# Performance work log

Measured on AMD Instinct MI355X. Metric: run time of the kernel, lower is better.

The kernel has to match this reference:

```python
import jax, jax.numpy as jnp
import numpy as np
import math

B, T = 32768, 34
VOCAB = 14
SQRT_HD = math.sqrt(3.0)

def _pos_flat_index():
    # flatten (source, index) pairs into indices of a [14,3] table:
    # rows 0-9 = digit spiral enc, row 10 = z10_enc, rows 11-13 = special_enc
    flat = []
    for p in range(34):
        if p < 10:
            flat.append(p)
        elif p == 10:
            flat.append(11 + 0)
        elif p < 21:
            flat.append(p - 11)
        elif p == 21:
            flat.append(11 + 1)
        elif p < 33:
            z = p - 22
            flat.append(z if z < 10 else 10)
        else:
            flat.append(11 + 2)
    return np.array(flat, dtype=np.int32)

POS_FLAT = _pos_flat_index()

def setup_inputs() -> dict:
    key = jax.random.key(0)
    ks = jax.random.split(key, 12)
    r = lambda k, s: jax.random.normal(k, s, dtype=jnp.float32)
    return {
        'idx': jax.random.randint(ks[0], (B, T), 0, VOCAB, dtype=jnp.int64),
        'tok_emb': r(ks[1], (14, 3)),
        'pos_params': r(ks[2], (4,)),
        'z10_enc': r(ks[3], (1, 3)),
        'special_enc': r(ks[4], (3, 3)),
        'wq': r(ks[5], (3, 6)), 'wk': r(ks[6], (3, 6)), 'wv': r(ks[7], (3, 6)),
        'wo': r(ks[8], (6, 6)),
        'ln1_g': jnp.ones(6), 'ln1_b': jnp.zeros(6),
        'ln2_g': jnp.ones(6), 'ln2_b': jnp.zeros(6),
        'lnf_g': jnp.ones(6), 'lnf_b': jnp.zeros(6),
        'ffn_w1': r(ks[9], (6, 2)), 'ffn_b1': jnp.zeros(2),
        'ffn_w2': r(ks[10], (2, 6)), 'ffn_b2': jnp.zeros(6),
        'head_w': r(ks[11], (6, 3)),
    }

def _ln(x, g, b):
    mu = x.mean(-1, keepdims=True)
    var = ((x - mu) ** 2).mean(-1, keepdims=True)
    return (x - mu) * jax.lax.rsqrt(var + 1e-5) * g + b

def _forward(idx, tok_emb, pos_params, z10_enc, special_enc, wq, wk, wv, wo,
             ln1_g, ln1_b, ln2_g, ln2_b, lnf_g, lnf_b,
             ffn_w1, ffn_b1, ffn_w2, ffn_b2, head_w):
    amp, phase, slope, offset = pos_params[0], pos_params[1], pos_params[2], pos_params[3]
    i = jnp.arange(10, dtype=jnp.float32)
    ang = 2.0 * math.pi * i / 10.0 + phase
    digit = jnp.stack([amp * jnp.cos(ang), amp * jnp.sin(ang), slope * i + offset], -1)  # [10,3]
    table = jnp.concatenate([digit, z10_enc, special_enc], 0)  # [14,3]
    Tn = idx.shape[1]
    pos = table[POS_FLAT][:Tn]  # [T,3]
    tok = tok_emb[idx]  # [B,T,3]
    x = jnp.concatenate([tok, jnp.broadcast_to(pos, tok.shape)], -1)  # [B,T,6]
    h = _ln(x, ln1_g, ln1_b)
    h_tok, h_pos = h[..., :3], h[..., 3:]
    Bn = idx.shape[0]
    q = (h_pos @ wq).reshape(Bn, Tn, 2, 3)
    k = (h_pos @ wk).reshape(Bn, Tn, 2, 3)
    v = (h_tok @ wv).reshape(Bn, Tn, 2, 3)
    attn = jnp.einsum('bqhd,bkhd->bhqk', q, k) / SQRT_HD
    mask = jnp.tril(jnp.ones((Tn, Tn), bool))
    attn = jax.nn.softmax(jnp.where(mask, attn, -jnp.inf), axis=-1)
    o = jnp.einsum('bhqk,bkhd->bqhd', attn, v).reshape(Bn, Tn, 6)
    x = x + o @ wo
    h2 = _ln(x, ln2_g, ln2_b)
    x = x + (jax.nn.gelu(h2 @ ffn_w1 + ffn_b1, approximate=False) @ ffn_w2 + ffn_b2)
    x = _ln(x, lnf_g, lnf_b)
    return (x @ head_w) @ tok_emb.T  # [B,T,14]

def reference(idx, tok_emb, pos_params, z10_enc, special_enc, wq, wk, wv, wo,
              ln1_g, ln1_b, ln2_g, ln2_b, lnf_g, lnf_b,
              ffn_w1, ffn_b1, ffn_w2, ffn_b2, head_w):
    return _forward(idx, tok_emb, pos_params, z10_enc, special_enc, wq, wk, wv, wo,
                    ln1_g, ln1_b, ln2_g, ln2_b, lnf_g, lnf_b,
                    ffn_w1, ffn_b1, ffn_w2, ffn_b2, head_w)
```

## Files before the change

### kernel.cpp

```cpp
#include <hip/hip_runtime.h>
#include <math.h>

#define BT    34
#define TPR   17
#define RPB   15
#define BLOCK 256

typedef float v2f __attribute__((ext_vector_type(2)));
typedef float v4f __attribute__((ext_vector_type(4)));

#define QSCALE 0.83294037332470f

#if __has_builtin(__builtin_amdgcn_exp2f)
#define EXP2(x) __builtin_amdgcn_exp2f(x)
#else
#define EXP2(x) exp2f(x)
#endif

__device__ __forceinline__ void ln6(const float* x, const float* g, const float* b, float* o) {
  float mu = (x[0]+x[1]+x[2]+x[3]+x[4]+x[5]) * (1.0f/6.0f);
  float v = 0.f;
  #pragma unroll
  for (int c = 0; c < 6; ++c) { float d = x[c]-mu; v += d*d; }
  float inv = rsqrtf(v * (1.0f/6.0f) + 1e-5f);
  #pragma unroll
  for (int c = 0; c < 6; ++c) o[c] = (x[c]-mu)*inv*g[c] + b[c];
}

__global__ __launch_bounds__(BLOCK, 4)
void addtrans_kernel(const int* __restrict__ idx,
                     const float* __restrict__ tok_emb,
                     const float* __restrict__ pos_params,
                     const float* __restrict__ z10_enc,
                     const float* __restrict__ special_enc,
                     const float* __restrict__ wq,
                     const float* __restrict__ wk,
                     const float* __restrict__ wv,
                     const float* __restrict__ wo,
                     const float* __restrict__ ln1_g, const float* __restrict__ ln1_b,
                     const float* __restrict__ ln2_g, const float* __restrict__ ln2_b,
                     const float* __restrict__ lnf_g, const float* __restrict__ lnf_b,
                     const float* __restrict__ ffn_w1, const float* __restrict__ ffn_b1,
                     const float* __restrict__ ffn_w2, const float* __restrict__ ffn_b2,
                     const float* __restrict__ head_w,
                     float* __restrict__ out, int B)
{
  __shared__ __align__(16) float s_mem[RPB*BT*14];
  __shared__ float s_te[42];
  __shared__ float s_pos[BT*3];
  __shared__ float s_wq[18], s_wk[18], s_wv[18], s_wo[36], s_hw[18];
  __shared__ float s_g1[6], s_b1[6], s_g2[6], s_b2[6], s_gf[6], s_bf[6];
  __shared__ float s_w1[12], s_w2[12], s_fb1[2], s_fb2[6];

  const int tid = threadIdx.x;

  if (tid < 42) s_te[tid] = tok_emb[tid];
  if (tid < 18) { s_wq[tid]=wq[tid]; s_wk[tid]=wk[tid]; s_wv[tid]=wv[tid]; s_hw[tid]=head_w[tid]; }
  if (tid < 36) s_wo[tid] = wo[tid];
  if (tid < 12) { s_w1[tid]=ffn_w1[tid]; s_w2[tid]=ffn_w2[tid]; }
  if (tid < 6)  { s_g1[tid]=ln1_g[tid]; s_b1[tid]=ln1_b[tid];
                  s_g2[tid]=ln2_g[tid]; s_b2[tid]=ln2_b[tid];
                  s_gf[tid]=lnf_g[tid]; s_bf[tid]=lnf_b[tid];
                  s_fb2[tid]=ffn_b2[tid]; }
  if (tid < 2)  s_fb1[tid] = ffn_b1[tid];
  if (tid < BT) {
    int p = tid, f;
    if (p < 10) f = p;
    else if (p == 10) f = 11;
    else if (p < 21) f = p - 11;
    else if (p == 21) f = 12;
    else if (p < 33) { int z = p - 22; f = (z < 10) ? z : 10; }
    else f = 13;
    float e0, e1, e2;
    if (f < 10) {
      float amp = pos_params[0], ph = pos_params[1], sl = pos_params[2], of = pos_params[3];
      float ang = 0.62831853071795864769f * (float)f + ph;
      e0 = amp * cosf(ang); e1 = amp * sinf(ang); e2 = sl * (float)f + of;
    } else if (f == 10) { e0 = z10_enc[0]; e1 = z10_enc[1]; e2 = z10_enc[2]; }
    else { int u = f - 11; e0 = special_enc[u*3]; e1 = special_enc[u*3+1]; e2 = special_enc[u*3+2]; }
    s_pos[tid*3+0] = e0; s_pos[tid*3+1] = e1; s_pos[tid*3+2] = e2;
  }
  __syncthreads();

  const int row = tid / TPR;
  const int j   = tid - row * TPR;
  const int b   = blockIdx.x * RPB + row;
  const bool active = (row < RPB) && (b < B);

  v2f   qp[2][3];
  float xr[2][6];

  if (active) {
    const int base = b * BT;
    #pragma unroll
    for (int s = 0; s < 2; ++s) {
      const int t = j + s * TPR;
      const int vid = idx[base + t];
      float x6[6];
      x6[0] = s_te[vid*3+0]; x6[1] = s_te[vid*3+1]; x6[2] = s_te[vid*3+2];
      x6[3] = s_pos[t*3+0];  x6[4] = s_pos[t*3+1];  x6[5] = s_pos[t*3+2];
      float h[6];
      ln6(x6, s_g1, s_b1, h);
      float q6[6], k6[6], v6[6];
      #pragma unroll
      for (int c = 0; c < 6; ++c) {
        q6[c] = h[3]*s_wq[c] + h[4]*s_wq[6+c] + h[5]*s_wq[12+c];
        k6[c] = h[3]*s_wk[c] + h[4]*s_wk[6+c] + h[5]*s_wk[12+c];
        v6[c] = h[0]*s_wv[c] + h[1]*s_wv[6+c] + h[2]*s_wv[12+c];
        xr[s][c] = x6[c];
      }
      qp[s][0] = (v2f){q6[0]*QSCALE, q6[3]*QSCALE};
      qp[s][1] = (v2f){q6[1]*QSCALE, q6[4]*QSCALE};
      qp[s][2] = (v2f){q6[2]*QSCALE, q6[5]*QSCALE};
      v4f* kvp = (v4f*)&s_mem[(row*BT + t)*12];
      kvp[0] = (v4f){k6[0], k6[3], k6[1], k6[4]};
      kvp[1] = (v4f){k6[2], k6[5], v6[0], v6[3]};
      kvp[2] = (v4f){v6[1], v6[4], v6[2], v6[5]};
    }
  }
  __syncthreads();

  v2f l0 = (v2f){0.f,0.f}, l1 = (v2f){0.f,0.f};
  v2f o0[3] = {(v2f){0.f,0.f},(v2f){0.f,0.f},(v2f){0.f,0.f}};
  v2f o1[3] = {(v2f){0.f,0.f},(v2f){0.f,0.f},(v2f){0.f,0.f}};
  if (active) {
    const v4f* kvb = (const v4f*)&s_mem[row * (BT*12)];
    #pragma unroll 4
    for (int k = 0; k < TPR; ++k) {
      v4f A = kvb[k*3+0], Bv = kvb[k*3+1], C = kvb[k*3+2];
      v2f kA = (v2f){A.x, A.y}, kB = (v2f){A.z, A.w}, kC = (v2f){Bv.x, Bv.y};
      v2f vA = (v2f){Bv.z, Bv.w}, vB = (v2f){C.x, C.y}, vC = (v2f){C.z, C.w};
      v2f s0 = qp[0][0]*kA + qp[0][1]*kB + qp[0][2]*kC;
      const float mf = (k <= j) ? 1.f : 0.f;
      v2f p0 = (v2f){EXP2(s0.x), EXP2(s0.y)};
      p0 *= mf;
      l0 += p0; o0[0] += p0*vA; o0[1] += p0*vB; o0[2] += p0*vC;
      v2f s1 = qp[1][0]*kA + qp[1][1]*kB + qp[1][2]*kC;
      v2f p1 = (v2f){EXP2(s1.x), EXP2(s1.y)};
      l1 += p1; o1[0] += p1*vA; o1[1] += p1*vB; o1[2] += p1*vC;
    }
    #pragma unroll 4
    for (int k = TPR; k < BT; ++k) {
      v4f A = kvb[k*3+0], Bv = kvb[k*3+1], C = kvb[k*3+2];
      v2f kA = (v2f){A.x, A.y}, kB = (v2f){A.z, A.w}, kC = (v2f){Bv.x, Bv.y};
      v2f vA = (v2f){Bv.z, Bv.w}, vB = (v2f){C.x, C.y}, vC = (v2f){C.z, C.w};
      v2f s1 = qp[1][0]*kA + qp[1][1]*kB + qp[1][2]*kC;
      const float mf = (k <= j + TPR) ? 1.f : 0.f;
      v2f p1 = (v2f){EXP2(s1.x), EXP2(s1.y)};
      p1 *= mf;
      l1 += p1; o1[0] += p1*vA; o1[1] += p1*vB; o1[2] += p1*vC;
    }
  }
  __syncthreads();

  if (active) {
    #pragma unroll
    for (int s = 0; s < 2; ++s) {
      const int t = j + s * TPR;
      const v2f  lv = s ? l1 : l0;
      const v2f* ov = s ? o1 : o0;
      const float ia = __builtin_amdgcn_rcpf(lv.x);
      const float ib = __builtin_amdgcn_rcpf(lv.y);
      float a6[6] = { ov[0].x*ia, ov[1].x*ia, ov[2].x*ia,
                      ov[0].y*ib, ov[1].y*ib, ov[2].y*ib };
      float xn[6];
      #pragma unroll
      for (int c = 0; c < 6; ++c) {
        xn[c] = xr[s][c]
              + a6[0]*s_wo[c]    + a6[1]*s_wo[6+c]  + a6[2]*s_wo[12+c]
              + a6[3]*s_wo[18+c] + a6[4]*s_wo[24+c] + a6[5]*s_wo[30+c];
      }
      float h2[6];
      ln6(xn, s_g2, s_b2, h2);
      float a0 = s_fb1[0], a1 = s_fb1[1];
      #pragma unroll
      for (int d = 0; d < 6; ++d) { a0 += h2[d]*s_w1[d*2]; a1 += h2[d]*s_w1[d*2+1]; }
      const float g0 = 0.5f*a0*(1.0f + erff(a0*0.70710678118654752440f));
      const float g1 = 0.5f*a1*(1.0f + erff(a1*0.70710678118654752440f));
      #pragma unroll
      for (int c = 0; c < 6; ++c) xn[c] += g0*s_w2[c] + g1*s_w2[6+c] + s_fb2[c];
      float xf[6];
      ln6(xn, s_gf, s_bf, xf);
      float y0 = 0.f, y1 = 0.f, y2 = 0.f;
      #pragma unroll
      for (int c = 0; c < 6; ++c) {
        y0 += xf[c]*s_hw[c*3+0]; y1 += xf[c]*s_hw[c*3+1]; y2 += xf[c]*s_hw[c*3+2];
      }
      v2f* lp = (v2f*)&s_mem[(row*BT + t)*14];
      #pragma unroll
      for (int u = 0; u < 7; ++u) {
        const int c0 = 2*u, c1 = 2*u+1;
        lp[u] = (v2f){ y0*s_te[c0*3+0] + y1*s_te[c0*3+1] + y2*s_te[c0*3+2],
                       y0*s_te[c1*3+0] + y1*s_te[c1*3+1] + y2*s_te[c1*3+2] };
      }
    }
  }
  __syncthreads();

  {
    const int b0 = blockIdx.x * RPB;
    int nrows = B - b0; if (nrows > RPB) nrows = RPB;
    if (nrows > 0) {
      const int n4 = nrows * (BT*14/4);
      v4f* dst = reinterpret_cast<v4f*>(out + (size_t)b0 * (BT*14));
      const v4f* src = reinterpret_cast<const v4f*>(s_mem);
      for (int i = tid; i < n4; i += BLOCK)
        __builtin_nontemporal_store(src[i], dst + i);
    }
  }
}

extern "C" void kernel_launch(void* const* d_in, const int* in_sizes, int n_in,
                              void* d_out, int out_size, void* d_ws, size_t ws_size,
                              hipStream_t stream) {
  const int B = in_sizes[0] / BT;
  const int grid = (B + RPB - 1) / RPB;
  addtrans_kernel<<<grid, BLOCK, 0, stream>>>(
      (const int*)d_in[0],   (const float*)d_in[1], (const float*)d_in[2],
      (const float*)d_in[3], (const float*)d_in[4], (const float*)d_in[5],
      (const float*)d_in[6], (const float*)d_in[7], (const float*)d_in[8],
      (const float*)d_in[9], (const float*)d_in[10], (const float*)d_in[11],
      (const float*)d_in[12], (const float*)d_in[13], (const float*)d_in[14],
      (const float*)d_in[15], (const float*)d_in[16], (const float*)d_in[17],
      (const float*)d_in[18], (const float*)d_in[19],
      (float*)d_out, B);
}
```

Before: 139.7 us.

## Assign four query tokens per thread with smaller blocks and staged indices

Result: slower. 150.9 us (+8.0%).

```diff
diff --git a/kernel.cpp b/kernel.cpp
--- a/kernel.cpp
+++ b/kernel.cpp
@@ -2,9 +2,9 @@
 #include <math.h>
 
 #define BT    34
-#define TPR   17
-#define RPB   15
-#define BLOCK 256
+#define TPR   9
+#define RPB   7
+#define BLOCK 64
 
 typedef float v2f __attribute__((ext_vector_type(2)));
 typedef float v4f __attribute__((ext_vector_type(4)));
@@ -27,7 +27,7 @@
   for (int c = 0; c < 6; ++c) o[c] = (x[c]-mu)*inv*g[c] + b[c];
 }
 
-__global__ __launch_bounds__(BLOCK, 4)
+__global__ __launch_bounds__(BLOCK, 2)
 void addtrans_kernel(const int* __restrict__ idx,
                      const float* __restrict__ tok_emb,
                      const float* __restrict__ pos_params,
@@ -46,6 +46,7 @@
                      float* __restrict__ out, int B)
 {
   __shared__ __align__(16) float s_mem[RPB*BT*14];
+  __shared__ int   s_idx[RPB*BT];
   __shared__ float s_te[42];
   __shared__ float s_pos[BT*3];
   __shared__ float s_wq[18], s_wk[18], s_wv[18], s_wo[36], s_hw[18];
@@ -53,6 +54,8 @@
   __shared__ float s_w1[12], s_w2[12], s_fb1[2], s_fb2[6];
 
   const int tid = threadIdx.x;
+  const int b0  = blockIdx.x * RPB;
+  int nrows = B - b0; if (nrows > RPB) nrows = RPB; if (nrows < 0) nrows = 0;
 
   if (tid < 42) s_te[tid] = tok_emb[tid];
   if (tid < 18) { s_wq[tid]=wq[tid]; s_wk[tid]=wk[tid]; s_wv[tid]=wv[tid]; s_hw[tid]=head_w[tid]; }
@@ -63,6 +66,7 @@
                   s_gf[tid]=lnf_g[tid]; s_bf[tid]=lnf_b[tid];
                   s_fb2[tid]=ffn_b2[tid]; }
   if (tid < 2)  s_fb1[tid] = ffn_b1[tid];
+  for (int i = tid; i < nrows*BT; i += BLOCK) s_idx[i] = idx[b0*BT + i];
   if (tid < BT) {
     int p = tid, f;
     if (p < 10) f = p;
@@ -84,21 +88,22 @@
 
   const int row = tid / TPR;
   const int j   = tid - row * TPR;
-  const int b   = blockIdx.x * RPB + row;
-  const bool active = (row < RPB) && (b < B);
-
-  v2f   qp[2][3];
-  float xr[2][6];
+  const bool active = (row < RPB) && (row < nrows);
+  const bool has3 = (j < 7);
+
+  v2f qp[4][3];
+  int vid[4];
+  int tok[4];
+  tok[0] = j; tok[1] = j + 9; tok[2] = j + 18; tok[3] = has3 ? (j + 27) : 33;
 
   if (active) {
-    const int base = b * BT;
     #pragma unroll
-    for (int s = 0; s < 2; ++s) {
-      const int t = j + s * TPR;
-      const int vid = idx[base + t];
+    for (int s = 0; s < 4; ++s) {
+      const int t = tok[s];
+      vid[s] = s_idx[row*BT + t];
       float x6[6];
-      x6[0] = s_te[vid*3+0]; x6[1] = s_te[vid*3+1]; x6[2] = s_te[vid*3+2];
-      x6[3] = s_pos[t*3+0];  x6[4] = s_pos[t*3+1];  x6[5] = s_pos[t*3+2];
+      x6[0] = s_te[vid[s]*3+0]; x6[1] = s_te[vid[s]*3+1]; x6[2] = s_te[vid[s]*3+2];
+      x6[3] = s_pos[t*3+0];     x6[4] = s_pos[t*3+1];     x6[5] = s_pos[t*3+2];
       float h[6];
       ln6(x6, s_g1, s_b1, h);
       float q6[6], k6[6], v6[6];
@@ -107,7 +112,6 @@
         q6[c] = h[3]*s_wq[c] + h[4]*s_wq[6+c] + h[5]*s_wq[12+c];
         k6[c] = h[3]*s_wk[c] + h[4]*s_wk[6+c] + h[5]*s_wk[12+c];
         v6[c] = h[0]*s_wv[c] + h[1]*s_wv[6+c] + h[2]*s_wv[12+c];
-        xr[s][c] = x6[c];
       }
       qp[s][0] = (v2f){q6[0]*QSCALE, q6[3]*QSCALE};
       qp[s][1] = (v2f){q6[1]*QSCALE, q6[4]*QSCALE};
@@ -120,53 +124,67 @@
   }
   __syncthreads();
 
-  v2f l0 = (v2f){0.f,0.f}, l1 = (v2f){0.f,0.f};
-  v2f o0[3] = {(v2f){0.f,0.f},(v2f){0.f,0.f},(v2f){0.f,0.f}};
-  v2f o1[3] = {(v2f){0.f,0.f},(v2f){0.f,0.f},(v2f){0.f,0.f}};
+  v2f l[4]; v2f o[4][3];
+  #pragma unroll
+  for (int s = 0; s < 4; ++s) {
+    l[s] = (v2f){0.f,0.f};
+    o[s][0] = (v2f){0.f,0.f}; o[s][1] = (v2f){0.f,0.f}; o[s][2] = (v2f){0.f,0.f};
+  }
+
+#define LOADKV \
+    v4f A = kvb[k*3+0], Bv = kvb[k*3+1], C = kvb[k*3+2]; \
+    v2f kA = (v2f){A.x, A.y}, kB = (v2f){A.z, A.w}, kC = (v2f){Bv.x, Bv.y}; \
+    v2f vA = (v2f){Bv.z, Bv.w}, vB = (v2f){C.x, C.y}, vC = (v2f){C.z, C.w};
+#define QSTEP(s, PRED) do { \
+    v2f sc = qp[s][0]*kA + qp[s][1]*kB + qp[s][2]*kC; \
+    v2f p = (v2f){EXP2(sc.x), EXP2(sc.y)}; \
+    if (!(PRED)) p = (v2f){0.f,0.f}; \
+    l[s] += p; o[s][0] += p*vA; o[s][1] += p*vB; o[s][2] += p*vC; \
+  } while(0)
+
   if (active) {
     const v4f* kvb = (const v4f*)&s_mem[row * (BT*12)];
-    #pragma unroll 4
-    for (int k = 0; k < TPR; ++k) {
-      v4f A = kvb[k*3+0], Bv = kvb[k*3+1], C = kvb[k*3+2];
-      v2f kA = (v2f){A.x, A.y}, kB = (v2f){A.z, A.w}, kC = (v2f){Bv.x, Bv.y};
-      v2f vA = (v2f){Bv.z, Bv.w}, vB = (v2f){C.x, C.y}, vC = (v2f){C.z, C.w};
-      v2f s0 = qp[0][0]*kA + qp[0][1]*kB + qp[0][2]*kC;
-      const float mf = (k <= j) ? 1.f : 0.f;
-      v2f p0 = (v2f){EXP2(s0.x), EXP2(s0.y)};
-      p0 *= mf;
-      l0 += p0; o0[0] += p0*vA; o0[1] += p0*vB; o0[2] += p0*vC;
-      v2f s1 = qp[1][0]*kA + qp[1][1]*kB + qp[1][2]*kC;
-      v2f p1 = (v2f){EXP2(s1.x), EXP2(s1.y)};
-      l1 += p1; o1[0] += p1*vA; o1[1] += p1*vB; o1[2] += p1*vC;
-    }
-    #pragma unroll 4
-    for (int k = TPR; k < BT; ++k) {
-      v4f A = kvb[k*3+0], Bv = kvb[k*3+1], C = kvb[k*3+2];
-      v2f kA = (v2f){A.x, A.y}, kB = (v2f){A.z, A.w}, kC = (v2f){Bv.x, Bv.y};
-      v2f vA = (v2f){Bv.z, Bv.w}, vB = (v2f){C.x, C.y}, vC = (v2f){C.z, C.w};
-      v2f s1 = qp[1][0]*kA + qp[1][1]*kB + qp[1][2]*kC;
-      const float mf = (k <= j + TPR) ? 1.f : 0.f;
-      v2f p1 = (v2f){EXP2(s1.x), EXP2(s1.y)};
-      p1 *= mf;
-      l1 += p1; o1[0] += p1*vA; o1[1] += p1*vB; o1[2] += p1*vC;
+    #pragma unroll 3
+    for (int k = 0; k < 9; ++k) {
+      LOADKV;
+      QSTEP(0, k <= j); QSTEP(1, true); QSTEP(2, true); QSTEP(3, true);
+    }
+    #pragma unroll 3
+    for (int k = 9; k < 18; ++k) {
+      LOADKV;
+      QSTEP(1, k <= j+9); QSTEP(2, true); QSTEP(3, true);
+    }
+    #pragma unroll 3
+    for (int k = 18; k < 27; ++k) {
+      LOADKV;
+      QSTEP(2, k <= j+18); QSTEP(3, true);
+    }
+    if (has3) {
+      #pragma unroll 3
+      for (int k = 27; k < BT; ++k) {
+        LOADKV;
+        QSTEP(3, k <= j+27);
+      }
     }
   }
   __syncthreads();
 
   if (active) {
     #pragma unroll
-    for (int s = 0; s < 2; ++s) {
-      const int t = j + s * TPR;
-      const v2f  lv = s ? l1 : l0;
-      const v2f* ov = s ? o1 : o0;
-      const float ia = __builtin_amdgcn_rcpf(lv.x);
-      const float ib = __builtin_amdgcn_rcpf(lv.y);
-      float a6[6] = { ov[0].x*ia, ov[1].x*ia, ov[2].x*ia,
-                      ov[0].y*ib, ov[1].y*ib, ov[2].y*ib };
+    for (int s = 0; s < 4; ++s) {
+      if (s == 3 && !has3) continue;
+      const int t = tok[s];
+      const float ia = __builtin_amdgcn_rcpf(l[s].x);
+      const float ib = __builtin_amdgcn_rcpf(l[s].y);
+      float a6[6] = { o[s][0].x*ia, o[s][1].x*ia, o[s][2].x*ia,
+                      o[s][0].y*ib, o[s][1].y*ib, o[s][2].y*ib };
       float xn[6];
+      float xr0 = s_te[vid[s]*3+0], xr1 = s_te[vid[s]*3+1], xr2 = s_te[vid[s]*3+2];
+      float xr3 = s_pos[t*3+0],     xr4 = s_pos[t*3+1],     xr5 = s_pos[t*3+2];
+      float xrv[6] = {xr0, xr1, xr2, xr3, xr4, xr5};
       #pragma unroll
       for (int c = 0; c < 6; ++c) {
-        xn[c] = xr[s][c]
+        xn[c] = xrv[c]
               + a6[0]*s_wo[c]    + a6[1]*s_wo[6+c]  + a6[2]*s_wo[12+c]
               + a6[3]*s_wo[18+c] + a6[4]*s_wo[24+c] + a6[5]*s_wo[30+c];
       }
@@ -197,16 +215,12 @@
   }
   __syncthreads();
 
-  {
-    const int b0 = blockIdx.x * RPB;
-    int nrows = B - b0; if (nrows > RPB) nrows = RPB;
-    if (nrows > 0) {
-      const int n4 = nrows * (BT*14/4);
-      v4f* dst = reinterpret_cast<v4f*>(out + (size_t)b0 * (BT*14));
-      const v4f* src = reinterpret_cast<const v4f*>(s_mem);
-      for (int i = tid; i < n4; i += BLOCK)
-        __builtin_nontemporal_store(src[i], dst + i);
-    }
+  if (nrows > 0) {
+    const int n4 = nrows * (BT*14/4);
+    v4f* dst = reinterpret_cast<v4f*>(out + (size_t)b0 * (BT*14));
+    const v4f* src = reinterpret_cast<const v4f*>(s_mem);
+    for (int i = tid; i < n4; i += BLOCK)
+      __builtin_nontemporal_store(src[i], dst + i);
   }
 }
 
```

## Halve shared memory via fp16 logit staging and split K/V passes

Applied to the files above, without the earlier changes.

Result: slower. 144.0 us (+3.1%).

```diff
diff --git a/kernel.cpp b/kernel.cpp
--- a/kernel.cpp
+++ b/kernel.cpp
@@ -8,6 +8,7 @@
 
 typedef float v2f __attribute__((ext_vector_type(2)));
 typedef float v4f __attribute__((ext_vector_type(4)));
+typedef _Float16 h2 __attribute__((ext_vector_type(2)));
 
 #define QSCALE 0.83294037332470f
 
@@ -27,7 +28,7 @@
   for (int c = 0; c < 6; ++c) o[c] = (x[c]-mu)*inv*g[c] + b[c];
 }
 
-__global__ __launch_bounds__(BLOCK, 4)
+__global__ __launch_bounds__(BLOCK, 6)
 void addtrans_kernel(const int* __restrict__ idx,
                      const float* __restrict__ tok_emb,
                      const float* __restrict__ pos_params,
@@ -45,13 +46,14 @@
                      const float* __restrict__ head_w,
                      float* __restrict__ out, int B)
 {
-  __shared__ __align__(16) float s_mem[RPB*BT*14];
+  __shared__ __align__(16) unsigned s_u32[RPB*BT*7];
   __shared__ float s_te[42];
   __shared__ float s_pos[BT*3];
   __shared__ float s_wq[18], s_wk[18], s_wv[18], s_wo[36], s_hw[18];
   __shared__ float s_g1[6], s_b1[6], s_g2[6], s_b2[6], s_gf[6], s_bf[6];
   __shared__ float s_w1[12], s_w2[12], s_fb1[2], s_fb2[6];
 
+  float* s_kvf = (float*)s_u32;
   const int tid = threadIdx.x;
 
   if (tid < 42) s_te[tid] = tok_emb[tid];
@@ -84,38 +86,48 @@
 
   const int row = tid / TPR;
   const int j   = tid - row * TPR;
-  const int b   = blockIdx.x * RPB + row;
+  const int b0  = blockIdx.x * RPB;
+  const int b   = b0 + row;
+  int nrows = B - b0; if (nrows > RPB) nrows = RPB; if (nrows < 0) nrows = 0;
   const bool active = (row < RPB) && (b < B);
 
   v2f   qp[2][3];
-  float xr[2][6];
+  float h1[6];
+  int   vid[2];
 
   if (active) {
     const int base = b * BT;
     #pragma unroll
     for (int s = 0; s < 2; ++s) {
       const int t = j + s * TPR;
-      const int vid = idx[base + t];
+      vid[s] = idx[base + t];
       float x6[6];
-      x6[0] = s_te[vid*3+0]; x6[1] = s_te[vid*3+1]; x6[2] = s_te[vid*3+2];
-      x6[3] = s_pos[t*3+0];  x6[4] = s_pos[t*3+1];  x6[5] = s_pos[t*3+2];
+      x6[0] = s_te[vid[s]*3+0]; x6[1] = s_te[vid[s]*3+1]; x6[2] = s_te[vid[s]*3+2];
+      x6[3] = s_pos[t*3+0];     x6[4] = s_pos[t*3+1];     x6[5] = s_pos[t*3+2];
       float h[6];
       ln6(x6, s_g1, s_b1, h);
-      float q6[6], k6[6], v6[6];
-      #pragma unroll
-      for (int c = 0; c < 6; ++c) {
+      float q6[6];
+      #pragma unroll
+      for (int c = 0; c < 6; ++c)
         q6[c] = h[3]*s_wq[c] + h[4]*s_wq[6+c] + h[5]*s_wq[12+c];
-        k6[c] = h[3]*s_wk[c] + h[4]*s_wk[6+c] + h[5]*s_wk[12+c];
-        v6[c] = h[0]*s_wv[c] + h[1]*s_wv[6+c] + h[2]*s_wv[12+c];
-        xr[s][c] = x6[c];
-      }
       qp[s][0] = (v2f){q6[0]*QSCALE, q6[3]*QSCALE};
       qp[s][1] = (v2f){q6[1]*QSCALE, q6[4]*QSCALE};
       qp[s][2] = (v2f){q6[2]*QSCALE, q6[5]*QSCALE};
-      v4f* kvp = (v4f*)&s_mem[(row*BT + t)*12];
-      kvp[0] = (v4f){k6[0], k6[3], k6[1], k6[4]};
-      kvp[1] = (v4f){k6[2], k6[5], v6[0], v6[3]};
-      kvp[2] = (v4f){v6[1], v6[4], v6[2], v6[5]};
+      if (s == 0) {
+        float k6[6], v6[6];
+        #pragma unroll
+        for (int c = 0; c < 6; ++c) {
+          k6[c] = h[3]*s_wk[c] + h[4]*s_wk[6+c] + h[5]*s_wk[12+c];
+          v6[c] = h[0]*s_wv[c] + h[1]*s_wv[6+c] + h[2]*s_wv[12+c];
+        }
+        v4f* kvp = (v4f*)&s_kvf[(row*TPR + j)*12];
+        kvp[0] = (v4f){k6[0], k6[3], k6[1], k6[4]};
+        kvp[1] = (v4f){k6[2], k6[5], v6[0], v6[3]};
+        kvp[2] = (v4f){v6[1], v6[4], v6[2], v6[5]};
+      } else {
+        #pragma unroll
+        for (int c = 0; c < 6; ++c) h1[c] = h[c];
+      }
     }
   }
   __syncthreads();
@@ -123,32 +135,48 @@
   v2f l0 = (v2f){0.f,0.f}, l1 = (v2f){0.f,0.f};
   v2f o0[3] = {(v2f){0.f,0.f},(v2f){0.f,0.f},(v2f){0.f,0.f}};
   v2f o1[3] = {(v2f){0.f,0.f},(v2f){0.f,0.f},(v2f){0.f,0.f}};
-  if (active) {
-    const v4f* kvb = (const v4f*)&s_mem[row * (BT*12)];
+  const v4f* kvb = (const v4f*)&s_kvf[row * (TPR*12)];
+
+#define LOADKV(kk) \
+    v4f A = kvb[(kk)*3+0], Bv = kvb[(kk)*3+1], C = kvb[(kk)*3+2]; \
+    v2f kA = (v2f){A.x, A.y}, kB = (v2f){A.z, A.w}, kC = (v2f){Bv.x, Bv.y}; \
+    v2f vA = (v2f){Bv.z, Bv.w}, vB = (v2f){C.x, C.y}, vC = (v2f){C.z, C.w};
+#define QSTEP(qq, ll, oo, PRED) do { \
+    v2f sc = qp[qq][0]*kA + qp[qq][1]*kB + qp[qq][2]*kC; \
+    v2f p = (v2f){EXP2(sc.x), EXP2(sc.y)}; \
+    if (!(PRED)) p = (v2f){0.f,0.f}; \
+    ll += p; oo[0] += p*vA; oo[1] += p*vB; oo[2] += p*vC; \
+  } while(0)
+
+  if (active) {
     #pragma unroll 4
     for (int k = 0; k < TPR; ++k) {
-      v4f A = kvb[k*3+0], Bv = kvb[k*3+1], C = kvb[k*3+2];
-      v2f kA = (v2f){A.x, A.y}, kB = (v2f){A.z, A.w}, kC = (v2f){Bv.x, Bv.y};
-      v2f vA = (v2f){Bv.z, Bv.w}, vB = (v2f){C.x, C.y}, vC = (v2f){C.z, C.w};
-      v2f s0 = qp[0][0]*kA + qp[0][1]*kB + qp[0][2]*kC;
-      const float mf = (k <= j) ? 1.f : 0.f;
-      v2f p0 = (v2f){EXP2(s0.x), EXP2(s0.y)};
-      p0 *= mf;
-      l0 += p0; o0[0] += p0*vA; o0[1] += p0*vB; o0[2] += p0*vC;
-      v2f s1 = qp[1][0]*kA + qp[1][1]*kB + qp[1][2]*kC;
-      v2f p1 = (v2f){EXP2(s1.x), EXP2(s1.y)};
-      l1 += p1; o1[0] += p1*vA; o1[1] += p1*vB; o1[2] += p1*vC;
-    }
+      LOADKV(k);
+      QSTEP(0, l0, o0, k <= j);
+      QSTEP(1, l1, o1, true);
+    }
+  }
+  __syncthreads();
+
+  if (active) {
+    float k6[6], v6[6];
+    #pragma unroll
+    for (int c = 0; c < 6; ++c) {
+      k6[c] = h1[3]*s_wk[c] + h1[4]*s_wk[6+c] + h1[5]*s_wk[12+c];
+      v6[c] = h1[0]*s_wv[c] + h1[1]*s_wv[6+c] + h1[2]*s_wv[12+c];
+    }
+    v4f* kvp = (v4f*)&s_kvf[(row*TPR + j)*12];
+    kvp[0] = (v4f){k6[0], k6[3], k6[1], k6[4]};
+    kvp[1] = (v4f){k6[2], k6[5], v6[0], v6[3]};
+    kvp[2] = (v4f){v6[1], v6[4], v6[2], v6[5]};
+  }
+  __syncthreads();
+
+  if (active) {
     #pragma unroll 4
-    for (int k = TPR; k < BT; ++k) {
-      v4f A = kvb[k*3+0], Bv = kvb[k*3+1], C = kvb[k*3+2];
-      v2f kA = (v2f){A.x, A.y}, kB = (v2f){A.z, A.w}, kC = (v2f){Bv.x, Bv.y};
-      v2f vA = (v2f){Bv.z, Bv.w}, vB = (v2f){C.x, C.y}, vC = (v2f){C.z, C.w};
-      v2f s1 = qp[1][0]*kA + qp[1][1]*kB + qp[1][2]*kC;
-      const float mf = (k <= j + TPR) ? 1.f : 0.f;
-      v2f p1 = (v2f){EXP2(s1.x), EXP2(s1.y)};
-      p1 *= mf;
-      l1 += p1; o1[0] += p1*vA; o1[1] += p1*vB; o1[2] += p1*vC;
+    for (int k2 = 0; k2 < TPR; ++k2) {
+      LOADKV(k2);
+      QSTEP(1, l1, o1, k2 <= j);
     }
   }
   __syncthreads();
@@ -164,17 +192,19 @@
       float a6[6] = { ov[0].x*ia, ov[1].x*ia, ov[2].x*ia,
                       ov[0].y*ib, ov[1].y*ib, ov[2].y*ib };
       float xn[6];
+      float xrv[6] = { s_te[vid[s]*3+0], s_te[vid[s]*3+1], s_te[vid[s]*3+2],
+                       s_pos[t*3+0],     s_pos[t*3+1],     s_pos[t*3+2] };
       #pragma unroll
       for (int c = 0; c < 6; ++c) {
-        xn[c] = xr[s][c]
+        xn[c] = xrv[c]
               + a6[0]*s_wo[c]    + a6[1]*s_wo[6+c]  + a6[2]*s_wo[12+c]
               + a6[3]*s_wo[18+c] + a6[4]*s_wo[24+c] + a6[5]*s_wo[30+c];
       }
-      float h2[6];
-      ln6(xn, s_g2, s_b2, h2);
+      float h2v[6];
+      ln6(xn, s_g2, s_b2, h2v);
       float a0 = s_fb1[0], a1 = s_fb1[1];
       #pragma unroll
-      for (int d = 0; d < 6; ++d) { a0 += h2[d]*s_w1[d*2]; a1 += h2[d]*s_w1[d*2+1]; }
+      for (int d = 0; d < 6; ++d) { a0 += h2v[d]*s_w1[d*2]; a1 += h2v[d]*s_w1[d*2+1]; }
       const float g0 = 0.5f*a0*(1.0f + erff(a0*0.70710678118654752440f));
       const float g1 = 0.5f*a1*(1.0f + erff(a1*0.70710678118654752440f));
       #pragma unroll
@@ -186,26 +216,25 @@
       for (int c = 0; c < 6; ++c) {
         y0 += xf[c]*s_hw[c*3+0]; y1 += xf[c]*s_hw[c*3+1]; y2 += xf[c]*s_hw[c*3+2];
       }
-      v2f* lp = (v2f*)&s_mem[(row*BT + t)*14];
+      unsigned* lp = &s_u32[(row*BT + t)*7];
       #pragma unroll
       for (int u = 0; u < 7; ++u) {
         const int c0 = 2*u, c1 = 2*u+1;
-        lp[u] = (v2f){ y0*s_te[c0*3+0] + y1*s_te[c0*3+1] + y2*s_te[c0*3+2],
-                       y0*s_te[c1*3+0] + y1*s_te[c1*3+1] + y2*s_te[c1*3+2] };
-      }
-    }
-  }
-  __syncthreads();
-
-  {
-    const int b0 = blockIdx.x * RPB;
-    int nrows = B - b0; if (nrows > RPB) nrows = RPB;
-    if (nrows > 0) {
-      const int n4 = nrows * (BT*14/4);
-      v4f* dst = reinterpret_cast<v4f*>(out + (size_t)b0 * (BT*14));
-      const v4f* src = reinterpret_cast<const v4f*>(s_mem);
-      for (int i = tid; i < n4; i += BLOCK)
-        __builtin_nontemporal_store(src[i], dst + i);
+        float f0 = y0*s_te[c0*3+0] + y1*s_te[c0*3+1] + y2*s_te[c0*3+2];
+        float f1 = y0*s_te[c1*3+0] + y1*s_te[c1*3+1] + y2*s_te[c1*3+2];
+        lp[u] = __builtin_bit_cast(unsigned, __builtin_amdgcn_cvt_pkrtz(f0, f1));
+      }
+    }
+  }
+  __syncthreads();
+
+  if (nrows > 0) {
+    const int n2 = nrows * (BT*14/2);
+    float* dst = out + (size_t)b0 * (BT*14);
+    for (int i = tid; i < n2; i += BLOCK) {
+      h2 hv = __builtin_bit_cast(h2, s_u32[i]);
+      v2f f = (v2f){(float)hv.x, (float)hv.y};
+      __builtin_nontemporal_store(f, (v2f*)(dst + 2*i));
     }
   }
 }
```
